# Optimization experiments

Measured on AMD Instinct MI355X. Metric: run time of the kernel, lower is better.

## Reference

```python
import jax, jax.numpy as jnp
import numpy as np

N_EXPERTS = 8
D_MODEL = 1024
D_FF = 2048
N_TOKENS = 4096
TOP_K = 2


def _init_expert_weight(key, shape):
    # matches torch init: bound = sqrt(3) * (sqrt(1/3)/sqrt(fan_in)) = 1/sqrt(fan_in)
    fan_in = shape[1]
    bound = 1.0 / np.sqrt(fan_in)
    return jax.random.uniform(key, shape, dtype=jnp.float32, minval=-bound, maxval=bound)


def setup_inputs() -> dict:
    key = jax.random.key(0)
    k_x, k_idx, k_w, k1, k2, k3 = jax.random.split(key, 6)
    x = jax.random.normal(k_x, (N_TOKENS, D_MODEL), dtype=jnp.float32)
    expert_indices = jax.random.randint(k_idx, (N_TOKENS, TOP_K), 0, N_EXPERTS)
    expert_weights = jax.random.uniform(k_w, (N_TOKENS, TOP_K), dtype=jnp.float32)
    w1 = _init_expert_weight(k1, (N_EXPERTS, D_MODEL, D_FF))
    w2 = _init_expert_weight(k2, (N_EXPERTS, D_MODEL, D_FF))
    w3 = _init_expert_weight(k3, (N_EXPERTS, D_FF, D_MODEL))
    return {"x": x, "expert_indices": expert_indices, "expert_weights": expert_weights,
            "w1": w1, "w2": w2, "w3": w3}


def reference(x, expert_indices, expert_weights, w1, w2, w3):
    # SwiGLU per expert, computed densely over all (token, expert) pairs,
    # then the top-k selected expert outputs are gathered and combined.
    # Mathematically identical to the padded-bmm dispatch/combine in the source.
    gate = jax.nn.silu(jnp.einsum('td,edf->tef', x, w1))   # [T, E, F]
    value = jnp.einsum('td,edf->tef', x, w2)               # [T, E, F]
    hidden = gate * value                                  # [T, E, F]
    out_e = jnp.einsum('tef,efd->ted', hidden, w3)         # [T, E, D]
    # gather each token's top-k expert outputs: [T, K, D]
    sel = jnp.take_along_axis(out_e, expert_indices[:, :, None], axis=1)
    return jnp.sum(sel * expert_weights[:, :, None], axis=1)  # [T, D]
```

## Files before the change

kernel.cpp:

```cpp
#include <hip/hip_runtime.h>
#include <hip/hip_bf16.h>

#define N_TOK   4096
#define DM      1024
#define DF      2048
#define NEXP    8
#define NPAIR   (N_TOK * 2)
#define BM      128
#define BN      128
#define BK      32
#define LDK     40

typedef __attribute__((ext_vector_type(8))) short bf16x8;
typedef __attribute__((ext_vector_type(4))) float f32x4;

__device__ __forceinline__ unsigned short to_bf16(float f) {
    unsigned u = __builtin_bit_cast(unsigned, f);
    unsigned r = (u + 0x7FFFu + ((u >> 16) & 1u)) >> 16;
    return (unsigned short)r;
}
__device__ __forceinline__ unsigned pk_bf16(float a, float b) {
    return (unsigned)to_bf16(a) | ((unsigned)to_bf16(b) << 16);
}
__device__ __forceinline__ void gld16(const unsigned short* g, unsigned short* l) {
    __builtin_amdgcn_global_load_lds(
        (const __attribute__((address_space(1))) unsigned int*)(g),
        (__attribute__((address_space(3))) unsigned int*)(l), 16, 0, 0);
}

__global__ void k_count(const int* __restrict__ eidx, int* __restrict__ meta) {
    int i = blockIdx.x * 256 + threadIdx.x;
    if (i < NPAIR) atomicAdd(&meta[eidx[i] & 7], 1);
}
__global__ void k_scan(int* __restrict__ meta) {
    if (threadIdx.x == 0) {
        int off = 0, mt = 0;
        for (int e = 0; e < NEXP; ++e) {
            meta[16 + e] = off; meta[25 + e] = mt;
            int c = meta[e];
            off += c; mt += (c + BM - 1) / BM;
        }
        meta[16 + NEXP] = off; meta[25 + NEXP] = mt; meta[34] = mt;
    }
}
__global__ void k_scatter(const int* __restrict__ eidx, int* __restrict__ meta,
                          int* __restrict__ rows) {
    int i = blockIdx.x * 256 + threadIdx.x;
    if (i < NPAIR) {
        int e = eidx[i] & 7;
        int p = meta[16 + e] + atomicAdd(&meta[8 + e], 1);
        rows[p] = i;
    }
}

__global__ __launch_bounds__(256)
void k_cvt_x(const float* __restrict__ x, unsigned short* __restrict__ xb) {
    int i = (blockIdx.x * 256 + threadIdx.x) * 8;
    float4 v0 = *(const float4*)(x + i);
    float4 v1 = *(const float4*)(x + i + 4);
    uint4 w;
    w.x = pk_bf16(v0.x, v0.y); w.y = pk_bf16(v0.z, v0.w);
    w.z = pk_bf16(v1.x, v1.y); w.w = pk_bf16(v1.z, v1.w);
    *(uint4*)(xb + i) = w;
}

__global__ __launch_bounds__(256)
void k_transpose(const float* __restrict__ src, unsigned short* __restrict__ dst,
                 int K, int F) {
    __shared__ __align__(16) unsigned short tile[64 * 80];
    const int e  = blockIdx.z;
    const int k0 = blockIdx.y * 64;
    const int f0 = blockIdx.x * 64;
    const int t  = threadIdx.x;
    const float* s = src + (size_t)e * K * F;
    unsigned short* d = dst + (size_t)e * K * F;
    const int fi = t & 63;
    const int kg = t >> 6;
    #pragma unroll
    for (int i = 0; i < 16; ++i) {
        int k = kg * 16 + i;
        tile[k * 80 + fi] = to_bf16(s[(size_t)(k0 + k) * F + f0 + fi]);
    }
    __syncthreads();
    const int kc = (t & 7) * 8;
    const int fo = t >> 3;
    #pragma unroll
    for (int j = 0; j < 2; ++j) {
        int f = fo + j * 32;
        unsigned short v[8];
        #pragma unroll
        for (int i = 0; i < 8; ++i) v[i] = tile[(kc + i) * 80 + f];
        uint4 w;
        w.x = (unsigned)v[0] | ((unsigned)v[1] << 16);
        w.y = (unsigned)v[2] | ((unsigned)v[3] << 16);
        w.z = (unsigned)v[4] | ((unsigned)v[5] << 16);
        w.w = (unsigned)v[6] | ((unsigned)v[7] << 16);
        *(uint4*)&d[(size_t)(f0 + f) * K + k0 + kc] = w;
    }
}

__global__ __launch_bounds__(256, 2)
void k_gemm1_bf(const unsigned short* __restrict__ xb,
                const unsigned short* __restrict__ w1t,
                const unsigned short* __restrict__ w2t,
                const int* __restrict__ meta,
                const int* __restrict__ rows,
                unsigned short* __restrict__ H)
{
    __shared__ __align__(16) unsigned short As [BM * BK];
    __shared__ __align__(16) unsigned short B1s[BN * BK];
    __shared__ __align__(16) unsigned short B2s[BN * BK];
    __shared__ int s_tok[BM];

    const int mt = blockIdx.y;
    if (mt >= meta[34]) return;
    int e = 0;
    #pragma unroll
    for (int i = 0; i < NEXP - 1; ++i) if (mt >= meta[25 + i + 1]) e = i + 1;
    const int rowEnd = meta[16 + e + 1];
    const int row0   = meta[16 + e] + (mt - meta[25 + e]) * BM;
    const int f0     = blockIdx.x * BN;
    const int tid    = threadIdx.x;

    if (tid < BM) {
        int gr = row0 + tid;
        s_tok[tid] = (gr < rowEnd) ? (rows[gr] >> 1) : 0;
    }
    __syncthreads();

    const int lane = tid & 63;
    const int wave = tid >> 6;
    const int r0 = wave * 32 + (lane >> 2);
    const int r1 = r0 + 16;
    const int kb = (lane & 3) * 8;
    const unsigned short* a_src0 = xb + (size_t)s_tok[r0] * DM + kb;
    const unsigned short* a_src1 = xb + (size_t)s_tok[r1] * DM + kb;
    const size_t wb = (size_t)e * DM * DF;
    const unsigned short* b1_src0 = w1t + wb + (size_t)(f0 + r0) * DM + kb;
    const unsigned short* b1_src1 = w1t + wb + (size_t)(f0 + r1) * DM + kb;
    const unsigned short* b2_src0 = w2t + wb + (size_t)(f0 + r0) * DM + kb;
    const unsigned short* b2_src1 = w2t + wb + (size_t)(f0 + r1) * DM + kb;
    unsigned short* As0  = &As [wave * 1024];
    unsigned short* As1  = &As [wave * 1024 + 512];
    unsigned short* B1s0 = &B1s[wave * 1024];
    unsigned short* B1s1 = &B1s[wave * 1024 + 512];
    unsigned short* B2s0 = &B2s[wave * 1024];
    unsigned short* B2s1 = &B2s[wave * 1024 + 512];

    f32x4 accg[4][4], accv[4][4];
    #pragma unroll
    for (int i = 0; i < 4; ++i)
        #pragma unroll
        for (int j = 0; j < 4; ++j) { accg[i][j] = (f32x4)0.f; accv[i][j] = (f32x4)0.f; }

    const int wm = (wave >> 1) * 64;
    const int wn = (wave & 1) * 64;
    const int am = lane & 15;
    const int ak = (lane >> 4) * 8;

    for (int k0 = 0; k0 < DM; k0 += BK) {
        gld16(a_src0 + k0, As0);
        gld16(a_src1 + k0, As1);
        gld16(b1_src0 + k0, B1s0);
        gld16(b1_src1 + k0, B1s1);
        gld16(b2_src0 + k0, B2s0);
        gld16(b2_src1 + k0, B2s1);
        __syncthreads();

        bf16x8 a[4], b1[4], b2[4];
        #pragma unroll
        for (int mi = 0; mi < 4; ++mi) a[mi] = *(const bf16x8*)&As[(wm + mi * 16 + am) * BK + ak];
        #pragma unroll
        for (int ni = 0; ni < 4; ++ni) {
            b1[ni] = *(const bf16x8*)&B1s[(wn + ni * 16 + am) * BK + ak];
            b2[ni] = *(const bf16x8*)&B2s[(wn + ni * 16 + am) * BK + ak];
        }
        #pragma unroll
        for (int mi = 0; mi < 4; ++mi)
            #pragma unroll
            for (int ni = 0; ni < 4; ++ni) {
                accg[mi][ni] = __builtin_amdgcn_mfma_f32_16x16x32_bf16(a[mi], b1[ni], accg[mi][ni], 0, 0, 0);
                accv[mi][ni] = __builtin_amdgcn_mfma_f32_16x16x32_bf16(a[mi], b2[ni], accv[mi][ni], 0, 0, 0);
            }
        __syncthreads();
    }

    const int cn = lane & 15;
    const int cq = (lane >> 4) * 4;
    #pragma unroll
    for (int mi = 0; mi < 4; ++mi) {
        #pragma unroll
        for (int r = 0; r < 4; ++r) {
            const int row = wm + mi * 16 + cq + r;
            const int gr  = row0 + row;
            if (gr < rowEnd) {
                unsigned short* dst = H + (size_t)gr * DF + f0 + wn;
                #pragma unroll
                for (int ni = 0; ni < 4; ++ni) {
                    float g = accg[mi][ni][r];
                    float v = accv[mi][ni][r];
                    float h = (g * v) / (1.f + __expf(-g));
                    dst[ni * 16 + cn] = to_bf16(h);
                }
            }
        }
    }
}

__global__ __launch_bounds__(256, 2)
void k_gemm2_bf(const unsigned short* __restrict__ H,
                const unsigned short* __restrict__ w3t,
                const int* __restrict__ meta,
                const int* __restrict__ rows,
                const float* __restrict__ ew,
                float* __restrict__ out)
{
    __shared__ __align__(16) unsigned short As[BM * BK];
    __shared__ __align__(16) unsigned short Bs[BN * BK];
    __shared__ int   s_tok[BM];
    __shared__ float s_w[BM];

    const int mt = blockIdx.y;
    if (mt >= meta[34]) return;
    int e = 0;
    #pragma unroll
    for (int i = 0; i < NEXP - 1; ++i) if (mt >= meta[25 + i + 1]) e = i + 1;
    const int rowEnd = meta[16 + e + 1];
    const int row0   = meta[16 + e] + (mt - meta[25 + e]) * BM;
    const int d0     = blockIdx.x * BN;
    const int tid    = threadIdx.x;

    if (tid < BM) {
        int gr = row0 + tid;
        if (gr < rowEnd) { int pr = rows[gr]; s_tok[tid] = pr >> 1; s_w[tid] = ew[pr]; }
        else             { s_tok[tid] = 0;    s_w[tid] = 0.f; }
    }
    __syncthreads();

    const int lane = tid & 63;
    const int wave = tid >> 6;
    const int r0 = wave * 32 + (lane >> 2);
    const int r1 = r0 + 16;
    const int kb = (lane & 3) * 8;
    int gr0 = row0 + r0; if (gr0 > NPAIR - 1) gr0 = NPAIR - 1;
    int gr1 = row0 + r1; if (gr1 > NPAIR - 1) gr1 = NPAIR - 1;
    const unsigned short* a_src0 = H + (size_t)gr0 * DF + kb;
    const unsigned short* a_src1 = H + (size_t)gr1 * DF + kb;
    const size_t wb = (size_t)e * DM * DF;
    const unsigned short* b_src0 = w3t + wb + (size_t)(d0 + r0) * DF + kb;
    const unsigned short* b_src1 = w3t + wb + (size_t)(d0 + r1) * DF + kb;
    unsigned short* As0 = &As[wave * 1024];
    unsigned short* As1 = &As[wave * 1024 + 512];
    unsigned short* Bs0 = &Bs[wave * 1024];
    unsigned short* Bs1 = &Bs[wave * 1024 + 512];

    f32x4 acc[4][4];
    #pragma unroll
    for (int i = 0; i < 4; ++i)
        #pragma unroll
        for (int j = 0; j < 4; ++j) acc[i][j] = (f32x4)0.f;

    const int wm = (wave >> 1) * 64;
    const int wn = (wave & 1) * 64;
    const int am = lane & 15;
    const int ak = (lane >> 4) * 8;

    for (int k0 = 0; k0 < DF; k0 += BK) {
        gld16(a_src0 + k0, As0);
        gld16(a_src1 + k0, As1);
        gld16(b_src0 + k0, Bs0);
        gld16(b_src1 + k0, Bs1);
        __syncthreads();

        bf16x8 a[4], b[4];
        #pragma unroll
        for (int mi = 0; mi < 4; ++mi) a[mi] = *(const bf16x8*)&As[(wm + mi * 16 + am) * BK + ak];
        #pragma unroll
        for (int ni = 0; ni < 4; ++ni) b[ni] = *(const bf16x8*)&Bs[(wn + ni * 16 + am) * BK + ak];
        #pragma unroll
        for (int mi = 0; mi < 4; ++mi)
            #pragma unroll
            for (int ni = 0; ni < 4; ++ni)
                acc[mi][ni] = __builtin_amdgcn_mfma_f32_16x16x32_bf16(a[mi], b[ni], acc[mi][ni], 0, 0, 0);
        __syncthreads();
    }

    const int cn = lane & 15;
    const int cq = (lane >> 4) * 4;
    #pragma unroll
    for (int mi = 0; mi < 4; ++mi) {
        #pragma unroll
        for (int r = 0; r < 4; ++r) {
            const int row = wm + mi * 16 + cq + r;
            const int gr  = row0 + row;
            if (gr < rowEnd) {
                const int   tok = s_tok[row];
                const float wgt = s_w[row];
                float* dst = out + (size_t)tok * DM + d0 + wn;
                #pragma unroll
                for (int ni = 0; ni < 4; ++ni)
                    atomicAdd(&dst[ni * 16 + cn], wgt * acc[mi][ni][r]);
            }
        }
    }
}

__global__ __launch_bounds__(256, 2)
void k_gemm1(const float* __restrict__ x, const float* __restrict__ w1,
             const float* __restrict__ w2, const int* __restrict__ meta,
             const int* __restrict__ rows, unsigned short* __restrict__ H)
{
    __shared__ unsigned short As[BM][LDK];
    __shared__ unsigned short B1s[BN][LDK];
    __shared__ unsigned short B2s[BN][LDK];
    __shared__ int s_tok[BM];
    const int mt = blockIdx.y;
    if (mt >= meta[34]) return;
    int e = 0;
    #pragma unroll
    for (int i = 0; i < NEXP - 1; ++i) if (mt >= meta[25 + i + 1]) e = i + 1;
    const int rowEnd = meta[16 + e + 1];
    const int row0   = meta[16 + e] + (mt - meta[25 + e]) * BM;
    const int f0     = blockIdx.x * BN;
    const int tid    = threadIdx.x;
    if (tid < BM) {
        int gr = row0 + tid;
        s_tok[tid] = (gr < rowEnd) ? (rows[gr] >> 1) : -1;
    }
    __syncthreads();
    const int ar = tid >> 1;
    const int ah = (tid & 1) * 16;
    const int a_tok = s_tok[ar];
    const float* a_src = x + (size_t)(a_tok < 0 ? 0 : a_tok) * DM + ah;
    const int bn_ = tid & 127;
    const int bk_ = (tid >> 7) * 16;
    const float* b1_src = w1 + (size_t)e * DM * DF + (size_t)bk_ * DF + f0 + bn_;
    const float* b2_src = w2 + (size_t)e * DM * DF + (size_t)bk_ * DF + f0 + bn_;
    f32x4 accg[4][4], accv[4][4];
    #pragma unroll
    for (int i = 0; i < 4; ++i)
        #pragma unroll
        for (int j = 0; j < 4; ++j) { accg[i][j] = (f32x4)0.f; accv[i][j] = (f32x4)0.f; }
    const int lane = tid & 63;
    const int wave = tid >> 6;
    const int wm = (wave >> 1) * 64;
    const int wn = (wave & 1) * 64;
    const int am = lane & 15;
    const int ak = (lane >> 4) * 8;
    for (int k0 = 0; k0 < DM; k0 += BK) {
        {
            const float* p = a_src + k0;
            #pragma unroll
            for (int jj = 0; jj < 4; ++jj) {
                float4 v;
                if (a_tok < 0) { v.x = v.y = v.z = v.w = 0.f; }
                else           { v = *(const float4*)(p + jj * 4); }
                uint2 w;
                w.x = pk_bf16(v.x, v.y); w.y = pk_bf16(v.z, v.w);
                *(uint2*)&As[ar][ah + jj * 4] = w;
            }
        }
        {
            const float* p1 = b1_src + (size_t)k0 * DF;
            const float* p2 = b2_src + (size_t)k0 * DF;
            #pragma unroll
            for (int c = 0; c < 2; ++c) {
                float v[8];
                #pragma unroll
                for (int j = 0; j < 8; ++j) v[j] = p1[(size_t)(c * 8 + j) * DF];
                uint4 w;
                w.x = pk_bf16(v[0], v[1]); w.y = pk_bf16(v[2], v[3]);
                w.z = pk_bf16(v[4], v[5]); w.w = pk_bf16(v[6], v[7]);
                *(uint4*)&B1s[bn_][bk_ + c * 8] = w;
            }
            #pragma unroll
            for (int c = 0; c < 2; ++c) {
                float v[8];
                #pragma unroll
                for (int j = 0; j < 8; ++j) v[j] = p2[(size_t)(c * 8 + j) * DF];
                uint4 w;
                w.x = pk_bf16(v[0], v[1]); w.y = pk_bf16(v[2], v[3]);
                w.z = pk_bf16(v[4], v[5]); w.w = pk_bf16(v[6], v[7]);
                *(uint4*)&B2s[bn_][bk_ + c * 8] = w;
            }
        }
        __syncthreads();
        bf16x8 a[4], b1[4], b2[4];
        #pragma unroll
        for (int mi = 0; mi < 4; ++mi) a[mi] = *(const bf16x8*)&As[wm + mi * 16 + am][ak];
        #pragma unroll
        for (int ni = 0; ni < 4; ++ni) {
            b1[ni] = *(const bf16x8*)&B1s[wn + ni * 16 + am][ak];
            b2[ni] = *(const bf16x8*)&B2s[wn + ni * 16 + am][ak];
        }
        #pragma unroll
        for (int mi = 0; mi < 4; ++mi)
            #pragma unroll
            for (int ni = 0; ni < 4; ++ni) {
                accg[mi][ni] = __builtin_amdgcn_mfma_f32_16x16x32_bf16(a[mi], b1[ni], accg[mi][ni], 0, 0, 0);
                accv[mi][ni] = __builtin_amdgcn_mfma_f32_16x16x32_bf16(a[mi], b2[ni], accv[mi][ni], 0, 0, 0);
            }
        __syncthreads();
    }
    const int cn = lane & 15;
    const int cq = (lane >> 4) * 4;
    #pragma unroll
    for (int mi = 0; mi < 4; ++mi) {
        #pragma unroll
        for (int r = 0; r < 4; ++r) {
            const int row = wm + mi * 16 + cq + r;
            const int gr  = row0 + row;
            if (gr < rowEnd) {
                unsigned short* dst = H + (size_t)gr * DF + f0 + wn;
                #pragma unroll
                for (int ni = 0; ni < 4; ++ni) {
                    float g = accg[mi][ni][r];
                    float v = accv[mi][ni][r];
                    float h = (g * v) / (1.f + __expf(-g));
                    dst[ni * 16 + cn] = to_bf16(h);
                }
            }
        }
    }
}

__global__ __launch_bounds__(256, 2)
void k_gemm2(const unsigned short* __restrict__ H, const float* __restrict__ w3,
             const int* __restrict__ meta, const int* __restrict__ rows,
             const float* __restrict__ ew, float* __restrict__ out)
{
    __shared__ unsigned short As[BM][LDK];
    __shared__ unsigned short Bs[BN][LDK];
    __shared__ int   s_tok[BM];
    __shared__ float s_w[BM];
    const int mt = blockIdx.y;
    if (mt >= meta[34]) return;
    int e = 0;
    #pragma unroll
    for (int i = 0; i < NEXP - 1; ++i) if (mt >= meta[25 + i + 1]) e = i + 1;
    const int rowEnd = meta[16 + e + 1];
    const int row0   = meta[16 + e] + (mt - meta[25 + e]) * BM;
    const int d0     = blockIdx.x * BN;
    const int tid    = threadIdx.x;
    if (tid < BM) {
        int gr = row0 + tid;
        if (gr < rowEnd) { int pr = rows[gr]; s_tok[tid] = pr >> 1; s_w[tid] = ew[pr]; }
        else             { s_tok[tid] = 0;    s_w[tid] = 0.f; }
    }
    __syncthreads();
    const int ar = tid >> 1;
    const int ah = (tid & 1) * 16;
    int a_row = row0 + ar; if (a_row >= NPAIR) a_row = NPAIR - 1;
    const unsigned short* a_src = H + (size_t)a_row * DF + ah;
    const int bn_ = tid & 127;
    const int bk_ = (tid >> 7) * 16;
    const float* b_src = w3 + (size_t)e * DF * DM + (size_t)bk_ * DM + d0 + bn_;
    f32x4 acc[4][4];
    #pragma unroll
    for (int i = 0; i < 4; ++i)
        #pragma unroll
        for (int j = 0; j < 4; ++j) acc[i][j] = (f32x4)0.f;
    const int lane = tid & 63;
    const int wave = tid >> 6;
    const int wm = (wave >> 1) * 64;
    const int wn = (wave & 1) * 64;
    const int am = lane & 15;
    const int ak = (lane >> 4) * 8;
    for (int k0 = 0; k0 < DF; k0 += BK) {
        *(uint4*)&As[ar][ah]     = *(const uint4*)(a_src + k0);
        *(uint4*)&As[ar][ah + 8] = *(const uint4*)(a_src + k0 + 8);
        {
            const float* p = b_src + (size_t)k0 * DM;
            #pragma unroll
            for (int c = 0; c < 2; ++c) {
                float v[8];
                #pragma unroll
                for (int j = 0; j < 8; ++j) v[j] = p[(size_t)(c * 8 + j) * DM];
                uint4 w;
                w.x = pk_bf16(v[0], v[1]); w.y = pk_bf16(v[2], v[3]);
                w.z = pk_bf16(v[4], v[5]); w.w = pk_bf16(v[6], v[7]);
                *(uint4*)&Bs[bn_][bk_ + c * 8] = w;
            }
        }
        __syncthreads();
        bf16x8 a[4], b[4];
        #pragma unroll
        for (int mi = 0; mi < 4; ++mi) a[mi] = *(const bf16x8*)&As[wm + mi * 16 + am][ak];
        #pragma unroll
        for (int ni = 0; ni < 4; ++ni) b[ni] = *(const bf16x8*)&Bs[wn + ni * 16 + am][ak];
        #pragma unroll
        for (int mi = 0; mi < 4; ++mi)
            #pragma unroll
            for (int ni = 0; ni < 4; ++ni)
                acc[mi][ni] = __builtin_amdgcn_mfma_f32_16x16x32_bf16(a[mi], b[ni], acc[mi][ni], 0, 0, 0);
        __syncthreads();
    }
    const int cn = lane & 15;
    const int cq = (lane >> 4) * 4;
    #pragma unroll
    for (int mi = 0; mi < 4; ++mi) {
        #pragma unroll
        for (int r = 0; r < 4; ++r) {
            const int row = wm + mi * 16 + cq + r;
            const int gr  = row0 + row;
            if (gr < rowEnd) {
                const int   tok = s_tok[row];
                const float wgt = s_w[row];
                float* dst = out + (size_t)tok * DM + d0 + wn;
                #pragma unroll
                for (int ni = 0; ni < 4; ++ni)
                    atomicAdd(&dst[ni * 16 + cn], wgt * acc[mi][ni][r]);
            }
        }
    }
}

__global__ __launch_bounds__(256)
void k_fallback(const float* __restrict__ x, const int* __restrict__ eidx,
                const float* __restrict__ ew, const float* __restrict__ w1,
                const float* __restrict__ w2, const float* __restrict__ w3,
                float* __restrict__ out)
{
    __shared__ float xs[DM];
    __shared__ float hs[DF];
    const int pair = blockIdx.x;
    const int t = pair >> 1;
    const int e = eidx[pair] & 7;
    const float wgt = ew[pair];
    const int tid = threadIdx.x;
    for (int i = tid; i < DM; i += 256) xs[i] = x[(size_t)t * DM + i];
    __syncthreads();
    for (int f = tid; f < DF; f += 256) {
        const float* c1 = w1 + (size_t)e * DM * DF + f;
        const float* c2 = w2 + (size_t)e * DM * DF + f;
        float g = 0.f, v = 0.f;
        for (int d = 0; d < DM; ++d) {
            float xv = xs[d];
            g += xv * c1[(size_t)d * DF];
            v += xv * c2[(size_t)d * DF];
        }
        hs[f] = (g * v) / (1.f + __expf(-g));
    }
    __syncthreads();
    for (int d = tid; d < DM; d += 256) {
        const float* c3 = w3 + (size_t)e * DF * DM + d;
        float o = 0.f;
        for (int f = 0; f < DF; ++f) o += hs[f] * c3[(size_t)f * DM];
        atomicAdd(&out[(size_t)t * DM + d], wgt * o);
    }
}

extern "C" void kernel_launch(void* const* d_in, const int* in_sizes, int n_in,
                              void* d_out, int out_size, void* d_ws, size_t ws_size,
                              hipStream_t stream)
{
    const float* x  = (const float*)d_in[0];
    const int*   ei = (const int*)  d_in[1];
    const float* ew = (const float*)d_in[2];
    const float* w1 = (const float*)d_in[3];
    const float* w2 = (const float*)d_in[4];
    const float* w3 = (const float*)d_in[5];
    float* out = (float*)d_out;

    (void)hipMemsetAsync(d_out, 0, (size_t)out_size * sizeof(float), stream);

    const size_t SZ_H  = (size_t)NPAIR * DF * 2;
    const size_t SZ_XB = (size_t)N_TOK * DM * 2;
    const size_t SZ_W  = (size_t)NEXP * DM * DF * 2;
    const size_t OFF_H  = 65536;
    const size_t OFF_XB = OFF_H + SZ_H;
    const size_t OFF_W1 = OFF_XB + SZ_XB;
    const size_t OFF_W2 = OFF_W1 + SZ_W;
    const size_t OFF_W3 = OFF_W2 + SZ_W;
    const size_t NEED_BIG   = OFF_W3 + SZ_W;
    const size_t NEED_SMALL = OFF_H + SZ_H;

    if (ws_size < NEED_SMALL) {
        k_fallback<<<NPAIR, 256, 0, stream>>>(x, ei, ew, w1, w2, w3, out);
        return;
    }

    int* meta = (int*)d_ws;
    int* rows = meta + 64;
    unsigned short* H = (unsigned short*)((char*)d_ws + OFF_H);

    (void)hipMemsetAsync(d_ws, 0, 64, stream);
    k_count  <<<NPAIR / 256, 256, 0, stream>>>(ei, meta);
    k_scan   <<<1, 64, 0, stream>>>(meta);
    k_scatter<<<NPAIR / 256, 256, 0, stream>>>(ei, meta, rows);

    if (ws_size >= NEED_BIG) {
        unsigned short* xb  = (unsigned short*)((char*)d_ws + OFF_XB);
        unsigned short* w1t = (unsigned short*)((char*)d_ws + OFF_W1);
        unsigned short* w2t = (unsigned short*)((char*)d_ws + OFF_W2);
        unsigned short* w3t = (unsigned short*)((char*)d_ws + OFF_W3);
        k_cvt_x<<<(N_TOK * DM) / 2048, 256, 0, stream>>>(x, xb);
        k_transpose<<<dim3(DF / 64, DM / 64, NEXP), 256, 0, stream>>>(w1, w1t, DM, DF);
        k_transpose<<<dim3(DF / 64, DM / 64, NEXP), 256, 0, stream>>>(w2, w2t, DM, DF);
        k_transpose<<<dim3(DM / 64, DF / 64, NEXP), 256, 0, stream>>>(w3, w3t, DF, DM);
        k_gemm1_bf<<<dim3(DF / BN, NPAIR / BM + NEXP), 256, 0, stream>>>(xb, w1t, w2t, meta, rows, H);
        k_gemm2_bf<<<dim3(DM / BN, NPAIR / BM + NEXP), 256, 0, stream>>>(H, w3t, meta, rows, ew, out);
    } else {
        k_gemm1<<<dim3(DF / BN, NPAIR / BM + NEXP), 256, 0, stream>>>(x, w1, w2, meta, rows, H);
        k_gemm2<<<dim3(DM / BN, NPAIR / BM + NEXP), 256, 0, stream>>>(H, w3, meta, rows, ew, out);
    }
}
```

Baseline: 493.2 us.

## Double-buffer LDS tiles in both expert GEMMs to overlap loads with MFMA

Both grouped GEMM kernels now keep two LDS buffers per operand. The next K-slice is prefetched with direct global-to-LDS loads while MFMAs run on the current slice, using explicit vmcnt waits and raw barriers in place of two __syncthreads per iteration. The goal is to hide global memory latency behind compute. In exchange, LDS use doubles, which may reduce occupancy at 2 blocks per CU, and the hand-counted vmcnt values are fragile if the number of loads per stage changes.

Result: no change. 495.4 us (+0.4%).

```diff
diff --git a/kernel.cpp b/kernel.cpp
--- a/kernel.cpp
+++ b/kernel.cpp
@@ -107,9 +107,9 @@
                 const int* __restrict__ rows,
                 unsigned short* __restrict__ H)
 {
-    __shared__ __align__(16) unsigned short As [BM * BK];
-    __shared__ __align__(16) unsigned short B1s[BN * BK];
-    __shared__ __align__(16) unsigned short B2s[BN * BK];
+    __shared__ __align__(16) unsigned short As [2][BM * BK];
+    __shared__ __align__(16) unsigned short B1s[2][BN * BK];
+    __shared__ __align__(16) unsigned short B2s[2][BN * BK];
     __shared__ int s_tok[BM];
 
     const int mt = blockIdx.y;
@@ -140,12 +140,6 @@
     const unsigned short* b1_src1 = w1t + wb + (size_t)(f0 + r1) * DM + kb;
     const unsigned short* b2_src0 = w2t + wb + (size_t)(f0 + r0) * DM + kb;
     const unsigned short* b2_src1 = w2t + wb + (size_t)(f0 + r1) * DM + kb;
-    unsigned short* As0  = &As [wave * 1024];
-    unsigned short* As1  = &As [wave * 1024 + 512];
-    unsigned short* B1s0 = &B1s[wave * 1024];
-    unsigned short* B1s1 = &B1s[wave * 1024 + 512];
-    unsigned short* B2s0 = &B2s[wave * 1024];
-    unsigned short* B2s1 = &B2s[wave * 1024 + 512];
 
     f32x4 accg[4][4], accv[4][4];
     #pragma unroll
@@ -158,22 +152,25 @@
     const int am = lane & 15;
     const int ak = (lane >> 4) * 8;
 
-    for (int k0 = 0; k0 < DM; k0 += BK) {
-        gld16(a_src0 + k0, As0);
-        gld16(a_src1 + k0, As1);
-        gld16(b1_src0 + k0, B1s0);
-        gld16(b1_src1 + k0, B1s1);
-        gld16(b2_src0 + k0, B2s0);
-        gld16(b2_src1 + k0, B2s1);
-        __syncthreads();
-
+    auto stage = [&](int bi, int k0) {
+        unsigned short* A0 = &As [bi][wave * 1024];
+        unsigned short* B1 = &B1s[bi][wave * 1024];
+        unsigned short* B2 = &B2s[bi][wave * 1024];
+        gld16(a_src0  + k0, A0);
+        gld16(a_src1  + k0, A0 + 512);
+        gld16(b1_src0 + k0, B1);
+        gld16(b1_src1 + k0, B1 + 512);
+        gld16(b2_src0 + k0, B2);
+        gld16(b2_src1 + k0, B2 + 512);
+    };
+    auto compute = [&](int bi) {
         bf16x8 a[4], b1[4], b2[4];
         #pragma unroll
-        for (int mi = 0; mi < 4; ++mi) a[mi] = *(const bf16x8*)&As[(wm + mi * 16 + am) * BK + ak];
+        for (int mi = 0; mi < 4; ++mi) a[mi] = *(const bf16x8*)&As[bi][(wm + mi * 16 + am) * BK + ak];
         #pragma unroll
         for (int ni = 0; ni < 4; ++ni) {
-            b1[ni] = *(const bf16x8*)&B1s[(wn + ni * 16 + am) * BK + ak];
-            b2[ni] = *(const bf16x8*)&B2s[(wn + ni * 16 + am) * BK + ak];
+            b1[ni] = *(const bf16x8*)&B1s[bi][(wn + ni * 16 + am) * BK + ak];
+            b2[ni] = *(const bf16x8*)&B2s[bi][(wn + ni * 16 + am) * BK + ak];
         }
         #pragma unroll
         for (int mi = 0; mi < 4; ++mi)
@@ -182,8 +179,24 @@
                 accg[mi][ni] = __builtin_amdgcn_mfma_f32_16x16x32_bf16(a[mi], b1[ni], accg[mi][ni], 0, 0, 0);
                 accv[mi][ni] = __builtin_amdgcn_mfma_f32_16x16x32_bf16(a[mi], b2[ni], accv[mi][ni], 0, 0, 0);
             }
-        __syncthreads();
-    }
+    };
+
+    stage(0, 0);
+    int cur = 0;
+    for (int t = 0; t < DM / BK - 1; ++t) {
+        stage(cur ^ 1, (t + 1) * BK);
+        asm volatile("s_waitcnt vmcnt(6)" ::: "memory");
+        __builtin_amdgcn_s_barrier();
+        __builtin_amdgcn_sched_barrier(0);
+        compute(cur);
+        __builtin_amdgcn_sched_barrier(0);
+        __builtin_amdgcn_s_barrier();
+        cur ^= 1;
+    }
+    asm volatile("s_waitcnt vmcnt(0)" ::: "memory");
+    __builtin_amdgcn_s_barrier();
+    __builtin_amdgcn_sched_barrier(0);
+    compute(cur);
 
     const int cn = lane & 15;
     const int cq = (lane >> 4) * 4;
@@ -215,8 +228,8 @@
                 const float* __restrict__ ew,
                 float* __restrict__ out)
 {
-    __shared__ __align__(16) unsigned short As[BM * BK];
-    __shared__ __align__(16) unsigned short Bs[BN * BK];
+    __shared__ __align__(16) unsigned short As[2][BM * BK];
+    __shared__ __align__(16) unsigned short Bs[2][BN * BK];
     __shared__ int   s_tok[BM];
     __shared__ float s_w[BM];
 
@@ -249,10 +262,6 @@
     const size_t wb = (size_t)e * DM * DF;
     const unsigned short* b_src0 = w3t + wb + (size_t)(d0 + r0) * DF + kb;
     const unsigned short* b_src1 = w3t + wb + (size_t)(d0 + r1) * DF + kb;
-    unsigned short* As0 = &As[wave * 1024];
-    unsigned short* As1 = &As[wave * 1024 + 512];
-    unsigned short* Bs0 = &Bs[wave * 1024];
-    unsigned short* Bs1 = &Bs[wave * 1024 + 512];
 
     f32x4 acc[4][4];
     #pragma unroll
@@ -265,25 +274,43 @@
     const int am = lane & 15;
     const int ak = (lane >> 4) * 8;
 
-    for (int k0 = 0; k0 < DF; k0 += BK) {
-        gld16(a_src0 + k0, As0);
-        gld16(a_src1 + k0, As1);
-        gld16(b_src0 + k0, Bs0);
-        gld16(b_src1 + k0, Bs1);
-        __syncthreads();
-
+    auto stage = [&](int bi, int k0) {
+        unsigned short* A0 = &As[bi][wave * 1024];
+        unsigned short* B0 = &Bs[bi][wave * 1024];
+        gld16(a_src0 + k0, A0);
+        gld16(a_src1 + k0, A0 + 512);
+        gld16(b_src0 + k0, B0);
+        gld16(b_src1 + k0, B0 + 512);
+    };
+    auto compute = [&](int bi) {
         bf16x8 a[4], b[4];
         #pragma unroll
-        for (int mi = 0; mi < 4; ++mi) a[mi] = *(const bf16x8*)&As[(wm + mi * 16 + am) * BK + ak];
-        #pragma unroll
-        for (int ni = 0; ni < 4; ++ni) b[ni] = *(const bf16x8*)&Bs[(wn + ni * 16 + am) * BK + ak];
+        for (int mi = 0; mi < 4; ++mi) a[mi] = *(const bf16x8*)&As[bi][(wm + mi * 16 + am) * BK + ak];
+        #pragma unroll
+        for (int ni = 0; ni < 4; ++ni) b[ni] = *(const bf16x8*)&Bs[bi][(wn + ni * 16 + am) * BK + ak];
         #pragma unroll
         for (int mi = 0; mi < 4; ++mi)
             #pragma unroll
             for (int ni = 0; ni < 4; ++ni)
                 acc[mi][ni] = __builtin_amdgcn_mfma_f32_16x16x32_bf16(a[mi], b[ni], acc[mi][ni], 0, 0, 0);
-        __syncthreads();
-    }
+    };
+
+    stage(0, 0);
+    int cur = 0;
+    for (int t = 0; t < DF / BK - 1; ++t) {
+        stage(cur ^ 1, (t + 1) * BK);
+        asm volatile("s_waitcnt vmcnt(4)" ::: "memory");
+        __builtin_amdgcn_s_barrier();
+        __builtin_amdgcn_sched_barrier(0);
+        compute(cur);
+        __builtin_amdgcn_sched_barrier(0);
+        __builtin_amdgcn_s_barrier();
+        cur ^= 1;
+    }
+    asm volatile("s_waitcnt vmcnt(0)" ::: "memory");
+    __builtin_amdgcn_s_barrier();
+    __builtin_amdgcn_sched_barrier(0);
+    compute(cur);
 
     const int cn = lane & 15;
     const int cq = (lane >> 4) * 4;
```
